# Kernel tuning notes

Measured on AMD Instinct MI355X. Metric: run time of the kernel, lower is better.

The kernel has to match this reference:

```python
import jax, jax.numpy as jnp
import numpy as np

NUM_HEADS = 16
HEAD_SIZE = 64
N_EMBED = 1024
BLOCK_SIZE = 1024
BATCH = 8


def setup_inputs() -> dict:
    key = jax.random.key(0)
    ks = jax.random.split(key, 8)
    s_in = 1.0 / np.sqrt(N_EMBED)
    x = jax.random.normal(ks[0], (BATCH, BLOCK_SIZE, N_EMBED), dtype=jnp.float32)
    Wq = jax.random.normal(ks[1], (N_EMBED, N_EMBED), dtype=jnp.float32) * s_in
    Wk = jax.random.normal(ks[2], (N_EMBED, N_EMBED), dtype=jnp.float32) * s_in
    Wv = jax.random.normal(ks[3], (N_EMBED, N_EMBED), dtype=jnp.float32) * s_in
    Wo = jax.random.normal(ks[4], (N_EMBED, N_EMBED), dtype=jnp.float32) * s_in
    bo = jnp.zeros((N_EMBED,), dtype=jnp.float32)
    W1 = jax.random.normal(ks[5], (N_EMBED, N_EMBED), dtype=jnp.float32) * s_in
    b1 = jnp.zeros((N_EMBED,), dtype=jnp.float32)
    return {"x": x, "Wq": Wq, "Wk": Wk, "Wv": Wv, "Wo": Wo, "bo": bo, "W1": W1, "b1": b1}


def reference(x, Wq, Wk, Wv, Wo, bo, W1, b1):
    B, T, E = x.shape
    H, Dh = NUM_HEADS, HEAD_SIZE
    # per-head projections (bias=False), concatenated weights reshaped to heads
    q = (x @ Wq).reshape(B, T, H, Dh)
    k = (x @ Wk).reshape(B, T, H, Dh)
    v = (x @ Wv).reshape(B, T, H, Dh)
    scale = Dh ** -0.5
    scores = jnp.einsum("bqhd,bkhd->bhqk", q, k) * scale  # [B,H,T,T]
    causal = jnp.tril(jnp.ones((T, T), dtype=bool))
    scores = jnp.where(causal, scores, jnp.float32(-jnp.inf))
    attn = jax.nn.softmax(scores, axis=-1)
    out = jnp.einsum("bhqk,bkhd->bqhd", attn, v).reshape(B, T, E)
    out = out @ Wo + bo  # output projection
    # FeedForward: Linear(E, E) + ReLU
    out = jax.nn.relu(out @ W1 + b1)
    return out
```

## Files before the change

### kernel.cpp

```cpp
#include <hip/hip_runtime.h>

typedef __bf16 bf16x8 __attribute__((ext_vector_type(8)));
typedef float f32x4 __attribute__((ext_vector_type(4)));
typedef short short4v __attribute__((ext_vector_type(4)));
typedef short short8v __attribute__((ext_vector_type(8)));

#define DEVI static __device__ __forceinline__

DEVI short f2bf(float f) {
    union { __bf16 b; short s; } u;
    u.b = (__bf16)f;
    return u.s;
}

DEVI void gld16(const void* g, void* l) {
    __builtin_amdgcn_global_load_lds(
        (const __attribute__((address_space(1))) unsigned int*)g,
        (__attribute__((address_space(3))) unsigned int*)l, 16, 0, 0);
}

__global__ __launch_bounds__(256) void cvt_x_kernel(const float* __restrict__ x,
                                                    short* __restrict__ xb) {
    int i = (blockIdx.x * 256 + threadIdx.x) * 8;
    f32x4 a = *(const f32x4*)(x + i);
    f32x4 b = *(const f32x4*)(x + i + 4);
    short8v o;
    o[0]=f2bf(a[0]); o[1]=f2bf(a[1]); o[2]=f2bf(a[2]); o[3]=f2bf(a[3]);
    o[4]=f2bf(b[0]); o[5]=f2bf(b[1]); o[6]=f2bf(b[2]); o[7]=f2bf(b[3]);
    *(short8v*)(xb + i) = o;
}

__global__ __launch_bounds__(256) void wtrans5_kernel(const float* __restrict__ w0,
                                                      const float* __restrict__ w1,
                                                      const float* __restrict__ w2,
                                                      const float* __restrict__ w3,
                                                      const float* __restrict__ w4,
                                                      short* __restrict__ dst) {
    const float* w;
    switch (blockIdx.z) {
        case 0: w = w0; break;
        case 1: w = w1; break;
        case 2: w = w2; break;
        case 3: w = w3; break;
        default: w = w4; break;
    }
    short* wt = dst + (size_t)blockIdx.z * 1048576;
    __shared__ float t[64][68];
    const int tid = threadIdx.x;
    const int k0 = blockIdx.x * 64, n0 = blockIdx.y * 64;
#pragma unroll
    for (int it = 0; it < 4; ++it) {
        int r = (tid >> 4) + it * 16;
        int cc = (tid & 15) * 4;
        f32x4 vv = *(const f32x4*)(w + (k0 + r) * 1024 + n0 + cc);
        *(f32x4*)&t[r][cc] = vv;
    }
    __syncthreads();
    if (blockIdx.z == 3) {
#pragma unroll
        for (int it = 0; it < 4; ++it) {
            int r = (tid >> 4) + it * 16;
            int cc = (tid & 15) * 4;
            short4v o;
            o[0] = f2bf(t[r][cc + 0]);
            o[1] = f2bf(t[r][cc + 1]);
            o[2] = f2bf(t[r][cc + 2]);
            o[3] = f2bf(t[r][cc + 3]);
            *(short4v*)(wt + (k0 + r) * 1024 + n0 + cc) = o;
        }
    } else {
#pragma unroll
        for (int it = 0; it < 4; ++it) {
            int n = (tid >> 4) + it * 16;
            int kc = (tid & 15) * 4;
            short4v o;
            o[0] = f2bf(t[kc + 0][n]);
            o[1] = f2bf(t[kc + 1][n]);
            o[2] = f2bf(t[kc + 2][n]);
            o[3] = f2bf(t[kc + 3][n]);
            *(short4v*)(wt + (n0 + n) * 1024 + k0 + kc) = o;
        }
    }
}

__global__ __launch_bounds__(256) void bcomb_kernel(const float* __restrict__ bo,
                                                    const float* __restrict__ W1,
                                                    const float* __restrict__ b1,
                                                    float* __restrict__ out) {
    __shared__ f32x4 red[64][4];
    const int tid = threadIdx.x;
    const int jg = tid >> 2;
    const int nq = tid & 3;
    const int n = blockIdx.x * 16 + nq * 4;
    f32x4 acc = {0.f, 0.f, 0.f, 0.f};
#pragma unroll 4
    for (int jj = 0; jj < 16; ++jj) {
        int j = jg * 16 + jj;
        float s = bo[j];
        f32x4 w = *(const f32x4*)(W1 + j * 1024 + n);
        acc[0] += s * w[0]; acc[1] += s * w[1]; acc[2] += s * w[2]; acc[3] += s * w[3];
    }
    red[jg][nq] = acc;
    __syncthreads();
#pragma unroll
    for (int s = 32; s >= 1; s >>= 1) {
        if (jg < s) {
            f32x4 a = red[jg][nq], b2 = red[jg + s][nq];
            a[0] += b2[0]; a[1] += b2[1]; a[2] += b2[2]; a[3] += b2[3];
            red[jg][nq] = a;
        }
        __syncthreads();
    }
    if (jg == 0) {
        f32x4 r = red[0][nq];
        f32x4 bb = *(const f32x4*)(b1 + n);
        r[0] += bb[0]; r[1] += bb[1]; r[2] += bb[2]; r[3] += bb[3];
        *(f32x4*)(out + n) = r;
    }
}

__global__ __launch_bounds__(256, 2) void gemm64_bt(const short* __restrict__ A,
                                                    const short* __restrict__ Bt,
                                                    short* __restrict__ outp) {
    __shared__ short As[64 * 64];
    __shared__ short Bs[64 * 64];
    const int tid = threadIdx.x;
    const int lane = tid & 63;
    const int wid = tid >> 6;
    const int g = lane >> 4, c = lane & 15;
    const int wr = wid >> 1, wc = wid & 1;
    const int m0 = blockIdx.x * 64, n0 = blockIdx.y * 64;

    const f32x4 fz = {0.f, 0.f, 0.f, 0.f};
    f32x4 acc[2][2];
#pragma unroll
    for (int m = 0; m < 2; ++m)
#pragma unroll
        for (int n = 0; n < 2; ++n) acc[m][n] = fz;

    for (int kt = 0; kt < 16; ++kt) {
        const int k0 = kt * 64;
        __syncthreads();
#pragma unroll
        for (int st = 0; st < 2; ++st) {
            int ci = st * 256 + tid;
            int r = ci >> 3;
            int cc = ((ci & 7) ^ (r & 7)) << 3;
            gld16(A + (m0 + r) * 1024 + k0 + cc, (char*)As + ci * 16);
            gld16(Bt + (n0 + r) * 1024 + k0 + cc, (char*)Bs + ci * 16);
        }
        __syncthreads();
#pragma unroll
        for (int kk = 0; kk < 2; ++kk) {
            bf16x8 af[2], bfr[2];
#pragma unroll
            for (int m = 0; m < 2; ++m) {
                int row = wr * 32 + m * 16 + c;
                af[m] = *(const bf16x8*)((const char*)As + row * 128 + ((kk * 64 + g * 16) ^ ((row & 7) << 4)));
            }
#pragma unroll
            for (int n = 0; n < 2; ++n) {
                int row = wc * 32 + n * 16 + c;
                bfr[n] = *(const bf16x8*)((const char*)Bs + row * 128 + ((kk * 64 + g * 16) ^ ((row & 7) << 4)));
            }
#pragma unroll
            for (int m = 0; m < 2; ++m)
#pragma unroll
                for (int n = 0; n < 2; ++n)
                    acc[m][n] = __builtin_amdgcn_mfma_f32_16x16x32_bf16(af[m], bfr[n], acc[m][n], 0, 0, 0);
        }
    }

#pragma unroll
    for (int n = 0; n < 2; ++n) {
        const int col = n0 + wc * 32 + n * 16 + c;
#pragma unroll
        for (int m = 0; m < 2; ++m) {
            const int row0 = m0 + wr * 32 + m * 16 + g * 4;
#pragma unroll
            for (int i = 0; i < 4; ++i)
                outp[(row0 + i) * 1024 + col] = f2bf(acc[m][n][i]);
        }
    }
}

template<int MODE>
__global__ __launch_bounds__(256, 2) void gemm_bt(const short* __restrict__ A,
                                                  const short* __restrict__ Bt,
                                                  const float* __restrict__ bias,
                                                  void* __restrict__ outp) {
    __shared__ short As[128 * 64];
    __shared__ short Bs[128 * 64];
    const int tid = threadIdx.x;
    const int lane = tid & 63;
    const int wid = tid >> 6;
    const int g = lane >> 4, c = lane & 15;
    const int wr = wid >> 1, wc = wid & 1;
    const int m0 = blockIdx.x * 128, n0 = blockIdx.y * 128;

    const f32x4 fz = {0.f, 0.f, 0.f, 0.f};
    f32x4 acc[4][4];
#pragma unroll
    for (int m = 0; m < 4; ++m)
#pragma unroll
        for (int n = 0; n < 4; ++n) acc[m][n] = fz;

    for (int kt = 0; kt < 16; ++kt) {
        const int k0 = kt * 64;
        __syncthreads();
#pragma unroll
        for (int st = 0; st < 4; ++st) {
            int ci = st * 256 + tid;
            int r = ci >> 3;
            int cc = ((ci & 7) ^ (r & 7)) << 3;
            gld16(A + (m0 + r) * 1024 + k0 + cc, (char*)As + ci * 16);
            gld16(Bt + (n0 + r) * 1024 + k0 + cc, (char*)Bs + ci * 16);
        }
        __syncthreads();
#pragma unroll
        for (int kk = 0; kk < 2; ++kk) {
            bf16x8 af[4], bfr[4];
#pragma unroll
            for (int m = 0; m < 4; ++m) {
                int row = wr * 64 + m * 16 + c;
                af[m] = *(const bf16x8*)((const char*)As + row * 128 + ((kk * 64 + g * 16) ^ ((row & 7) << 4)));
            }
#pragma unroll
            for (int n = 0; n < 4; ++n) {
                int row = wc * 64 + n * 16 + c;
                bfr[n] = *(const bf16x8*)((const char*)Bs + row * 128 + ((kk * 64 + g * 16) ^ ((row & 7) << 4)));
            }
#pragma unroll
            for (int m = 0; m < 4; ++m)
#pragma unroll
                for (int n = 0; n < 4; ++n)
                    acc[m][n] = __builtin_amdgcn_mfma_f32_16x16x32_bf16(af[m], bfr[n], acc[m][n], 0, 0, 0);
        }
    }

#pragma unroll
    for (int n = 0; n < 4; ++n) {
        const int col = n0 + wc * 64 + n * 16 + c;
        float bv = 0.f;
        if (MODE == 2) bv = bias[col];
#pragma unroll
        for (int m = 0; m < 4; ++m) {
            const int row0 = m0 + wr * 64 + m * 16 + g * 4;
#pragma unroll
            for (int i = 0; i < 4; ++i) {
                const int row = row0 + i;
                float val = acc[m][n][i];
                if (MODE == 0) {
                    short* qkv = (short*)outp;
                    int which = col >> 10;
                    int hc = col & 1023;
                    if (which == 0) val *= 0.18033688011112042f;
                    int dst = which * 8388608 +
                              (((row >> 10) * 16 + (hc >> 6)) * 1024 + (row & 1023)) * 64 + (hc & 63);
                    qkv[dst] = f2bf(val);
                } else {
                    ((float*)outp)[row * 1024 + col] = fmaxf(val + bv, 0.f);
                }
            }
        }
    }
}

__global__ __launch_bounds__(512, 2) void attn_kernel(const short* __restrict__ qp,
                                                      const short* __restrict__ kp,
                                                      const short* __restrict__ vp,
                                                      short* __restrict__ ao) {
    __shared__ short Ks[128 * 64];
    __shared__ short Vt[64 * 128];
    __shared__ short Ps[8][16 * 64];
    const int tid = threadIdx.x;
    const int lane = tid & 63;
    const int wid = tid >> 6;
    const int g = lane >> 4, c = lane & 15;
    const int bh = blockIdx.y;
    const int base = bh * 65536;
    const int b = bh >> 4, h = bh & 15;

    const int r0 = tid >> 3, c0 = (tid & 7) << 3;
    const int r1 = 64 + r0;
    const int vt0 = (tid >> 4) * 4;
    const int vd0 = (tid & 15) * 4;

    const f32x4 fz = {0.f, 0.f, 0.f, 0.f};

    bf16x8 kreg0, kreg1;
    short4v vreg0, vreg1, vreg2, vreg3;

#pragma unroll 1
    for (int ph = 0; ph < 2; ++ph) {
        const int qt = ph ? (7 - blockIdx.x) : blockIdx.x;
        const int q0 = qt * 128;
        const int nkt = qt + 1;

        const int qrow = q0 + wid * 16 + c;
        bf16x8 qf0 = *(const bf16x8*)(qp + base + qrow * 64 + g * 8);
        bf16x8 qf1 = *(const bf16x8*)(qp + base + qrow * 64 + 32 + g * 8);

        f32x4 accO[4];
#pragma unroll
        for (int n = 0; n < 4; ++n) accO[n] = fz;
        float mrow[4], lsum[4];
#pragma unroll
        for (int i = 0; i < 4; ++i) { mrow[i] = -1e30f; lsum[i] = 0.f; }

        kreg0 = *(const bf16x8*)(kp + base + r0 * 64 + c0);
        kreg1 = *(const bf16x8*)(kp + base + r1 * 64 + c0);
        vreg0 = *(const short4v*)(vp + base + (vt0 + 0) * 64 + vd0);
        vreg1 = *(const short4v*)(vp + base + (vt0 + 1) * 64 + vd0);
        vreg2 = *(const short4v*)(vp + base + (vt0 + 2) * 64 + vd0);
        vreg3 = *(const short4v*)(vp + base + (vt0 + 3) * 64 + vd0);

        for (int kt = 0; kt < nkt; ++kt) {
            __syncthreads();
            *(bf16x8*)((char*)Ks + r0 * 128 + ((c0 * 2) ^ ((r0 & 7) << 4))) = kreg0;
            *(bf16x8*)((char*)Ks + r1 * 128 + ((c0 * 2) ^ ((r1 & 7) << 4))) = kreg1;
#pragma unroll
            for (int i = 0; i < 4; ++i) {
                short4v w; w[0] = vreg0[i]; w[1] = vreg1[i]; w[2] = vreg2[i]; w[3] = vreg3[i];
                int d = vd0 + i;
                int swz = ((d & 7) ^ (d >> 3)) << 4;
                *(short4v*)((char*)Vt + d * 256 + ((vt0 * 2) ^ swz)) = w;
            }
            if (kt + 1 < nkt) {
                const short* kp2 = kp + base + (kt + 1) * 8192;
                const short* vp2 = vp + base + (kt + 1) * 8192;
                kreg0 = *(const bf16x8*)(kp2 + r0 * 64 + c0);
                kreg1 = *(const bf16x8*)(kp2 + r1 * 64 + c0);
                vreg0 = *(const short4v*)(vp2 + (vt0 + 0) * 64 + vd0);
                vreg1 = *(const short4v*)(vp2 + (vt0 + 1) * 64 + vd0);
                vreg2 = *(const short4v*)(vp2 + (vt0 + 2) * 64 + vd0);
                vreg3 = *(const short4v*)(vp2 + (vt0 + 3) * 64 + vd0);
            }
            __syncthreads();

            const bool diag = (kt == nkt - 1);
            const int nlim = diag ? (wid + 1) : 8;

            f32x4 s[8];
            __builtin_amdgcn_s_setprio(1);
#pragma unroll
            for (int n = 0; n < 8; ++n) {
                s[n] = fz;
                if (n < nlim) {
                    int row = n * 16 + c;
                    int swz = (row & 7) << 4;
                    bf16x8 kf0 = *(const bf16x8*)((const char*)Ks + row * 128 + ((g * 16) ^ swz));
                    bf16x8 kf1 = *(const bf16x8*)((const char*)Ks + row * 128 + ((64 + g * 16) ^ swz));
                    s[n] = __builtin_amdgcn_mfma_f32_16x16x32_bf16(qf0, kf0, s[n], 0, 0, 0);
                    s[n] = __builtin_amdgcn_mfma_f32_16x16x32_bf16(qf1, kf1, s[n], 0, 0, 0);
                }
            }
            __builtin_amdgcn_s_setprio(0);

            const int qg0 = q0 + wid * 16 + g * 4;
            float pm[4];
#pragma unroll
            for (int i = 0; i < 4; ++i) pm[i] = -1e30f;
            if (diag) {
#pragma unroll
                for (int n = 0; n < 8; ++n) {
                    int kg = kt * 128 + n * 16 + c;
#pragma unroll
                    for (int i = 0; i < 4; ++i) {
                        float vv = s[n][i];
                        vv = (kg <= qg0 + i) ? vv : -1e30f;
                        s[n][i] = vv;
                        pm[i] = fmaxf(pm[i], vv);
                    }
                }
            } else {
#pragma unroll
                for (int n = 0; n < 8; ++n)
#pragma unroll
                    for (int i = 0; i < 4; ++i)
                        pm[i] = fmaxf(pm[i], s[n][i]);
            }
#pragma unroll
            for (int off = 1; off < 16; off <<= 1)
#pragma unroll
                for (int i = 0; i < 4; ++i)
                    pm[i] = fmaxf(pm[i], __shfl_xor(pm[i], off));

            int need = 0;
#pragma unroll
            for (int i = 0; i < 4; ++i) need |= (pm[i] > mrow[i] + 8.f) ? 1 : 0;
            if (__any(need)) {
#pragma unroll
                for (int i = 0; i < 4; ++i) {
                    float mnew = fmaxf(mrow[i], pm[i]);
                    float corr = exp2f(mrow[i] - mnew);
                    mrow[i] = mnew;
                    lsum[i] *= corr;
#pragma unroll
                    for (int n = 0; n < 4; ++n) accO[n][i] *= corr;
                }
            }
#pragma unroll
            for (int n = 0; n < 8; ++n)
#pragma unroll
                for (int i = 0; i < 4; ++i) {
                    float pv = exp2f(s[n][i] - mrow[i]);
                    s[n][i] = pv;
                    lsum[i] += pv;
                }

#pragma unroll
            for (int hf = 0; hf < 2; ++hf) {
                asm volatile("s_waitcnt lgkmcnt(0)" ::: "memory");
                __builtin_amdgcn_sched_barrier(0);
#pragma unroll
                for (int n4 = 0; n4 < 4; ++n4) {
                    int tl = n4 * 16 + c;
#pragma unroll
                    for (int i = 0; i < 4; ++i) {
                        int q = g * 4 + i;
                        *(short*)((char*)&Ps[wid][0] + q * 128 + ((tl * 2) ^ ((q & 7) << 4))) =
                            f2bf(s[hf * 4 + n4][i]);
                    }
                }
                asm volatile("s_waitcnt lgkmcnt(0)" ::: "memory");
                __builtin_amdgcn_sched_barrier(0);
#pragma unroll
                for (int ksl = 0; ksl < 2; ++ksl) {
                    const int ks = hf * 2 + ksl;
                    bf16x8 paf = *(const bf16x8*)((const char*)&Ps[wid][0] +
                                                  c * 128 + ((ksl * 64 + g * 16) ^ ((c & 7) << 4)));
                    __builtin_amdgcn_s_setprio(1);
#pragma unroll
                    for (int n = 0; n < 4; ++n) {
                        int d = n * 16 + c;
                        int swz = ((d & 7) ^ (d >> 3)) << 4;
                        bf16x8 vf = *(const bf16x8*)((const char*)Vt + d * 256 + ((ks * 64 + g * 16) ^ swz));
                        accO[n] = __builtin_amdgcn_mfma_f32_16x16x32_bf16(paf, vf, accO[n], 0, 0, 0);
                    }
                    __builtin_amdgcn_s_setprio(0);
                }
            }
        }

        float lrow[4];
#pragma unroll
        for (int i = 0; i < 4; ++i) lrow[i] = lsum[i];
#pragma unroll
        for (int off = 1; off < 16; off <<= 1)
#pragma unroll
            for (int i = 0; i < 4; ++i)
                lrow[i] += __shfl_xor(lrow[i], off);
        float inv[4];
#pragma unroll
        for (int i = 0; i < 4; ++i) inv[i] = __builtin_amdgcn_rcpf(lrow[i]);
#pragma unroll
        for (int n = 0; n < 4; ++n)
#pragma unroll
            for (int i = 0; i < 4; ++i) {
                int t = q0 + wid * 16 + g * 4 + i;
                float o = accO[n][i] * inv[i];
                ao[(b * 1024 + t) * 1024 + h * 64 + n * 16 + c] = f2bf(o);
            }
    }
}

extern "C" void kernel_launch(void* const* d_in, const int* in_sizes, int n_in,
                              void* d_out, int out_size, void* d_ws, size_t ws_size,
                              hipStream_t stream) {
    const float* x  = (const float*)d_in[0];
    const float* Wq = (const float*)d_in[1];
    const float* Wk = (const float*)d_in[2];
    const float* Wv = (const float*)d_in[3];
    const float* Wo = (const float*)d_in[4];
    const float* bo = (const float*)d_in[5];
    const float* W1 = (const float*)d_in[6];
    const float* b1 = (const float*)d_in[7];

    char* ws = (char*)d_ws;
    short* xb    = (short*)(ws + 0);
    short* wallT = (short*)(ws + 16777216);
    short* qb    = (short*)(ws + 27262976);
    short* kb    = qb + 8388608;
    short* vb    = qb + 16777216;
    short* ao    = xb;
    short* wqkvT = wallT;
    short* woBF  = wallT + 3145728;
    short* w1T   = wallT + 4194304;
    short* wcombT= wqkvT;
    float* bcomb = (float*)(ws + 16777216 + 2097152);

    cvt_x_kernel<<<4096, 256, 0, stream>>>(x, xb);
    wtrans5_kernel<<<dim3(16, 16, 5), 256, 0, stream>>>(Wq, Wk, Wv, Wo, W1, wallT);

    gemm_bt<0><<<dim3(64, 24), 256, 0, stream>>>(xb, wqkvT, nullptr, (void*)qb);
    gemm64_bt<<<dim3(16, 16), 256, 0, stream>>>(w1T, woBF, wcombT);
    bcomb_kernel<<<64, 256, 0, stream>>>(bo, W1, b1, bcomb);
    attn_kernel<<<dim3(4, 128), 512, 0, stream>>>(qb, kb, vb, ao);
    gemm_bt<2><<<dim3(64, 8), 256, 0, stream>>>(ao, wcombT, bcomb, d_out);
}
```

Baseline: 167.5 us.

## Restructure attention to 4 waves with 32 query rows each and 64-key tiles

The attention kernel moves from 8 waves of 16 query rows to 4 waves of 32 query rows, and from 128-key tiles to 64-key tiles. Each K/V fragment read from LDS is now reused across two MFMA row groups, which lowers LDS traffic per FLOP, and the finer key tiles trim wasted work on the causal diagonal. The cost is more accumulator registers per lane, fewer waves per block, and twice as many barrier-synchronised tile iterations.

New measurement: 172.6 us. 3.0% more time.

```diff
diff --git a/kernel.cpp b/kernel.cpp
--- a/kernel.cpp
+++ b/kernel.cpp
@@ -266,13 +266,13 @@
     }
 }
 
-__global__ __launch_bounds__(512, 2) void attn_kernel(const short* __restrict__ qp,
+__global__ __launch_bounds__(256, 2) void attn_kernel(const short* __restrict__ qp,
                                                       const short* __restrict__ kp,
                                                       const short* __restrict__ vp,
                                                       short* __restrict__ ao) {
-    __shared__ short Ks[128 * 64];
-    __shared__ short Vt[64 * 128];
-    __shared__ short Ps[8][16 * 64];
+    __shared__ short Ks[64 * 64];
+    __shared__ short Vt[64 * 64];
+    __shared__ short Ps[4][32 * 64];
     const int tid = threadIdx.x;
     const int lane = tid & 63;
     const int wid = tid >> 6;
@@ -282,7 +282,6 @@
     const int b = bh >> 4, h = bh & 15;
 
     const int r0 = tid >> 3, c0 = (tid & 7) << 3;
-    const int r1 = 64 + r0;
     const int vt0 = (tid >> 4) * 4;
     const int vd0 = (tid & 15) * 4;
 
@@ -295,21 +294,29 @@
     for (int ph = 0; ph < 2; ++ph) {
         const int qt = ph ? (7 - blockIdx.x) : blockIdx.x;
         const int q0 = qt * 128;
-        const int nkt = qt + 1;
-
-        const int qrow = q0 + wid * 16 + c;
-        bf16x8 qf0 = *(const bf16x8*)(qp + base + qrow * 64 + g * 8);
-        bf16x8 qf1 = *(const bf16x8*)(qp + base + qrow * 64 + 32 + g * 8);
-
-        f32x4 accO[4];
-#pragma unroll
-        for (int n = 0; n < 4; ++n) accO[n] = fz;
-        float mrow[4], lsum[4];
-#pragma unroll
-        for (int i = 0; i < 4; ++i) { mrow[i] = -1e30f; lsum[i] = 0.f; }
+        const int nkt = (qt + 1) * 2;
+        const int qlo = q0 + wid * 32;
+
+        bf16x8 qf[2][2];
+#pragma unroll
+        for (int m = 0; m < 2; ++m)
+#pragma unroll
+            for (int hh = 0; hh < 2; ++hh)
+                qf[m][hh] = *(const bf16x8*)(qp + base + (qlo + m * 16 + c) * 64 + hh * 32 + g * 8);
+
+        f32x4 accO[2][4];
+#pragma unroll
+        for (int m = 0; m < 2; ++m)
+#pragma unroll
+            for (int n = 0; n < 4; ++n) accO[m][n] = fz;
+        float mrow[2][4], lsum[2][4];
+#pragma unroll
+        for (int m = 0; m < 2; ++m)
+#pragma unroll
+            for (int i = 0; i < 4; ++i) { mrow[m][i] = -1e30f; lsum[m][i] = 0.f; }
 
         kreg0 = *(const bf16x8*)(kp + base + r0 * 64 + c0);
-        kreg1 = *(const bf16x8*)(kp + base + r1 * 64 + c0);
+        kreg1 = *(const bf16x8*)(kp + base + (r0 + 32) * 64 + c0);
         vreg0 = *(const short4v*)(vp + base + (vt0 + 0) * 64 + vd0);
         vreg1 = *(const short4v*)(vp + base + (vt0 + 1) * 64 + vd0);
         vreg2 = *(const short4v*)(vp + base + (vt0 + 2) * 64 + vd0);
@@ -318,19 +325,18 @@
         for (int kt = 0; kt < nkt; ++kt) {
             __syncthreads();
             *(bf16x8*)((char*)Ks + r0 * 128 + ((c0 * 2) ^ ((r0 & 7) << 4))) = kreg0;
-            *(bf16x8*)((char*)Ks + r1 * 128 + ((c0 * 2) ^ ((r1 & 7) << 4))) = kreg1;
+            *(bf16x8*)((char*)Ks + (r0 + 32) * 128 + ((c0 * 2) ^ ((r0 & 7) << 4))) = kreg1;
 #pragma unroll
             for (int i = 0; i < 4; ++i) {
                 short4v w; w[0] = vreg0[i]; w[1] = vreg1[i]; w[2] = vreg2[i]; w[3] = vreg3[i];
                 int d = vd0 + i;
-                int swz = ((d & 7) ^ (d >> 3)) << 4;
-                *(short4v*)((char*)Vt + d * 256 + ((vt0 * 2) ^ swz)) = w;
+                *(short4v*)((char*)Vt + d * 128 + ((vt0 * 2) ^ ((d & 7) << 4))) = w;
             }
             if (kt + 1 < nkt) {
-                const short* kp2 = kp + base + (kt + 1) * 8192;
-                const short* vp2 = vp + base + (kt + 1) * 8192;
+                const short* kp2 = kp + base + (kt + 1) * 4096;
+                const short* vp2 = vp + base + (kt + 1) * 4096;
                 kreg0 = *(const bf16x8*)(kp2 + r0 * 64 + c0);
-                kreg1 = *(const bf16x8*)(kp2 + r1 * 64 + c0);
+                kreg1 = *(const bf16x8*)(kp2 + (r0 + 32) * 64 + c0);
                 vreg0 = *(const short4v*)(vp2 + (vt0 + 0) * 64 + vd0);
                 vreg1 = *(const short4v*)(vp2 + (vt0 + 1) * 64 + vd0);
                 vreg2 = *(const short4v*)(vp2 + (vt0 + 2) * 64 + vd0);
@@ -338,130 +344,165 @@
             }
             __syncthreads();
 
-            const bool diag = (kt == nkt - 1);
-            const int nlim = diag ? (wid + 1) : 8;
-
-            f32x4 s[8];
-            __builtin_amdgcn_s_setprio(1);
-#pragma unroll
-            for (int n = 0; n < 8; ++n) {
-                s[n] = fz;
-                if (n < nlim) {
-                    int row = n * 16 + c;
-                    int swz = (row & 7) << 4;
-                    bf16x8 kf0 = *(const bf16x8*)((const char*)Ks + row * 128 + ((g * 16) ^ swz));
-                    bf16x8 kf1 = *(const bf16x8*)((const char*)Ks + row * 128 + ((64 + g * 16) ^ swz));
-                    s[n] = __builtin_amdgcn_mfma_f32_16x16x32_bf16(qf0, kf0, s[n], 0, 0, 0);
-                    s[n] = __builtin_amdgcn_mfma_f32_16x16x32_bf16(qf1, kf1, s[n], 0, 0, 0);
-                }
-            }
-            __builtin_amdgcn_s_setprio(0);
-
-            const int qg0 = q0 + wid * 16 + g * 4;
-            float pm[4];
-#pragma unroll
-            for (int i = 0; i < 4; ++i) pm[i] = -1e30f;
-            if (diag) {
-#pragma unroll
-                for (int n = 0; n < 8; ++n) {
-                    int kg = kt * 128 + n * 16 + c;
-#pragma unroll
-                    for (int i = 0; i < 4; ++i) {
-                        float vv = s[n][i];
-                        vv = (kg <= qg0 + i) ? vv : -1e30f;
-                        s[n][i] = vv;
-                        pm[i] = fmaxf(pm[i], vv);
+            const int klo = kt * 64;
+            const bool skip = klo > qlo + 31;
+            if (!skip) {
+                const bool needMask = (klo + 63 > qlo);
+                int nlim = 4;
+                if (needMask) {
+                    nlim = ((qlo + 31 - klo) >> 4) + 1;
+                    if (nlim > 4) nlim = 4;
+                }
+
+                f32x4 s[2][4];
+#pragma unroll
+                for (int m = 0; m < 2; ++m)
+#pragma unroll
+                    for (int n = 0; n < 4; ++n) s[m][n] = fz;
+                __builtin_amdgcn_s_setprio(1);
+#pragma unroll
+                for (int n = 0; n < 4; ++n) {
+                    if (n < nlim) {
+                        int row = n * 16 + c;
+                        int swz = (c & 7) << 4;
+                        bf16x8 kf0 = *(const bf16x8*)((const char*)Ks + row * 128 + ((g * 16) ^ swz));
+                        bf16x8 kf1 = *(const bf16x8*)((const char*)Ks + row * 128 + ((64 + g * 16) ^ swz));
+#pragma unroll
+                        for (int m = 0; m < 2; ++m) {
+                            s[m][n] = __builtin_amdgcn_mfma_f32_16x16x32_bf16(qf[m][0], kf0, s[m][n], 0, 0, 0);
+                            s[m][n] = __builtin_amdgcn_mfma_f32_16x16x32_bf16(qf[m][1], kf1, s[m][n], 0, 0, 0);
+                        }
                     }
                 }
-            } else {
-#pragma unroll
-                for (int n = 0; n < 8; ++n)
+                __builtin_amdgcn_s_setprio(0);
+
+                float pm[2][4];
+#pragma unroll
+                for (int m = 0; m < 2; ++m)
+#pragma unroll
+                    for (int i = 0; i < 4; ++i) pm[m][i] = -1e30f;
+                if (needMask) {
+#pragma unroll
+                    for (int n = 0; n < 4; ++n) {
+                        int kg = klo + n * 16 + c;
+#pragma unroll
+                        for (int m = 0; m < 2; ++m)
+#pragma unroll
+                            for (int i = 0; i < 4; ++i) {
+                                float vv = s[m][n][i];
+                                vv = (kg <= qlo + m * 16 + g * 4 + i) ? vv : -1e30f;
+                                s[m][n][i] = vv;
+                                pm[m][i] = fmaxf(pm[m][i], vv);
+                            }
+                    }
+                } else {
+#pragma unroll
+                    for (int n = 0; n < 4; ++n)
+#pragma unroll
+                        for (int m = 0; m < 2; ++m)
+#pragma unroll
+                            for (int i = 0; i < 4; ++i)
+                                pm[m][i] = fmaxf(pm[m][i], s[m][n][i]);
+                }
+#pragma unroll
+                for (int off = 1; off < 16; off <<= 1)
+#pragma unroll
+                    for (int m = 0; m < 2; ++m)
+#pragma unroll
+                        for (int i = 0; i < 4; ++i)
+                            pm[m][i] = fmaxf(pm[m][i], __shfl_xor(pm[m][i], off));
+
+                int need = 0;
+#pragma unroll
+                for (int m = 0; m < 2; ++m)
 #pragma unroll
                     for (int i = 0; i < 4; ++i)
-                        pm[i] = fmaxf(pm[i], s[n][i]);
-            }
-#pragma unroll
-            for (int off = 1; off < 16; off <<= 1)
-#pragma unroll
-                for (int i = 0; i < 4; ++i)
-                    pm[i] = fmaxf(pm[i], __shfl_xor(pm[i], off));
-
-            int need = 0;
-#pragma unroll
-            for (int i = 0; i < 4; ++i) need |= (pm[i] > mrow[i] + 8.f) ? 1 : 0;
-            if (__any(need)) {
-#pragma unroll
-                for (int i = 0; i < 4; ++i) {
-                    float mnew = fmaxf(mrow[i], pm[i]);
-                    float corr = exp2f(mrow[i] - mnew);
-                    mrow[i] = mnew;
-                    lsum[i] *= corr;
-#pragma unroll
-                    for (int n = 0; n < 4; ++n) accO[n][i] *= corr;
-                }
-            }
-#pragma unroll
-            for (int n = 0; n < 8; ++n)
-#pragma unroll
-                for (int i = 0; i < 4; ++i) {
-                    float pv = exp2f(s[n][i] - mrow[i]);
-                    s[n][i] = pv;
-                    lsum[i] += pv;
-                }
-
-#pragma unroll
-            for (int hf = 0; hf < 2; ++hf) {
+                        need |= (pm[m][i] > mrow[m][i] + 8.f) ? 1 : 0;
+                if (__any(need)) {
+#pragma unroll
+                    for (int m = 0; m < 2; ++m)
+#pragma unroll
+                        for (int i = 0; i < 4; ++i) {
+                            float mnew = fmaxf(mrow[m][i], pm[m][i]);
+                            float corr = exp2f(mrow[m][i] - mnew);
+                            mrow[m][i] = mnew;
+                            lsum[m][i] *= corr;
+#pragma unroll
+                            for (int n = 0; n < 4; ++n) accO[m][n][i] *= corr;
+                        }
+                }
+#pragma unroll
+                for (int m = 0; m < 2; ++m)
+#pragma unroll
+                    for (int n = 0; n < 4; ++n)
+#pragma unroll
+                        for (int i = 0; i < 4; ++i) {
+                            float pv = exp2f(s[m][n][i] - mrow[m][i]);
+                            s[m][n][i] = pv;
+                            lsum[m][i] += pv;
+                        }
+
                 asm volatile("s_waitcnt lgkmcnt(0)" ::: "memory");
                 __builtin_amdgcn_sched_barrier(0);
 #pragma unroll
-                for (int n4 = 0; n4 < 4; ++n4) {
-                    int tl = n4 * 16 + c;
-#pragma unroll
-                    for (int i = 0; i < 4; ++i) {
-                        int q = g * 4 + i;
-                        *(short*)((char*)&Ps[wid][0] + q * 128 + ((tl * 2) ^ ((q & 7) << 4))) =
-                            f2bf(s[hf * 4 + n4][i]);
+                for (int m = 0; m < 2; ++m)
+#pragma unroll
+                    for (int n = 0; n < 4; ++n) {
+                        int t = n * 16 + c;
+#pragma unroll
+                        for (int i = 0; i < 4; ++i) {
+                            int q = m * 16 + g * 4 + i;
+                            *(short*)((char*)&Ps[wid][0] + q * 128 + ((t * 2) ^ ((q & 7) << 4))) =
+                                f2bf(s[m][n][i]);
+                        }
                     }
-                }
                 asm volatile("s_waitcnt lgkmcnt(0)" ::: "memory");
                 __builtin_amdgcn_sched_barrier(0);
-#pragma unroll
-                for (int ksl = 0; ksl < 2; ++ksl) {
-                    const int ks = hf * 2 + ksl;
-                    bf16x8 paf = *(const bf16x8*)((const char*)&Ps[wid][0] +
-                                                  c * 128 + ((ksl * 64 + g * 16) ^ ((c & 7) << 4)));
+
+#pragma unroll
+                for (int kk = 0; kk < 2; ++kk) {
+                    bf16x8 paf[2];
+#pragma unroll
+                    for (int m = 0; m < 2; ++m)
+                        paf[m] = *(const bf16x8*)((const char*)&Ps[wid][0] +
+                                                  (m * 16 + c) * 128 + ((kk * 64 + g * 16) ^ ((c & 7) << 4)));
                     __builtin_amdgcn_s_setprio(1);
 #pragma unroll
                     for (int n = 0; n < 4; ++n) {
                         int d = n * 16 + c;
-                        int swz = ((d & 7) ^ (d >> 3)) << 4;
-                        bf16x8 vf = *(const bf16x8*)((const char*)Vt + d * 256 + ((ks * 64 + g * 16) ^ swz));
-                        accO[n] = __builtin_amdgcn_mfma_f32_16x16x32_bf16(paf, vf, accO[n], 0, 0, 0);
+                        bf16x8 vf = *(const bf16x8*)((const char*)Vt + d * 128 +
+                                                     ((kk * 64 + g * 16) ^ ((d & 7) << 4)));
+#pragma unroll
+                        for (int m = 0; m < 2; ++m)
+                            accO[m][n] = __builtin_amdgcn_mfma_f32_16x16x32_bf16(paf[m], vf, accO[m][n], 0, 0, 0);
                     }
                     __builtin_amdgcn_s_setprio(0);
                 }
             }
         }
 
-        float lrow[4];
-#pragma unroll
-        for (int i = 0; i < 4; ++i) lrow[i] = lsum[i];
-#pragma unroll
-        for (int off = 1; off < 16; off <<= 1)
-#pragma unroll
-            for (int i = 0; i < 4; ++i)
-                lrow[i] += __shfl_xor(lrow[i], off);
-        float inv[4];
-#pragma unroll
-        for (int i = 0; i < 4; ++i) inv[i] = __builtin_amdgcn_rcpf(lrow[i]);
-#pragma unroll
-        for (int n = 0; n < 4; ++n)
-#pragma unroll
-            for (int i = 0; i < 4; ++i) {
-                int t = q0 + wid * 16 + g * 4 + i;
-                float o = accO[n][i] * inv[i];
-                ao[(b * 1024 + t) * 1024 + h * 64 + n * 16 + c] = f2bf(o);
-            }
+#pragma unroll
+        for (int m = 0; m < 2; ++m) {
+            float lrow[4];
+#pragma unroll
+            for (int i = 0; i < 4; ++i) lrow[i] = lsum[m][i];
+#pragma unroll
+            for (int off = 1; off < 16; off <<= 1)
+#pragma unroll
+                for (int i = 0; i < 4; ++i)
+                    lrow[i] += __shfl_xor(lrow[i], off);
+            float inv[4];
+#pragma unroll
+            for (int i = 0; i < 4; ++i) inv[i] = __builtin_amdgcn_rcpf(lrow[i]);
+#pragma unroll
+            for (int n = 0; n < 4; ++n)
+#pragma unroll
+                for (int i = 0; i < 4; ++i) {
+                    int t = qlo + m * 16 + g * 4 + i;
+                    float o = accO[m][n][i] * inv[i];
+                    ao[(b * 1024 + t) * 1024 + h * 64 + n * 16 + c] = f2bf(o);
+                }
+        }
     }
 }
 
@@ -496,6 +537,6 @@
     gemm_bt<0><<<dim3(64, 24), 256, 0, stream>>>(xb, wqkvT, nullptr, (void*)qb);
     gemm64_bt<<<dim3(16, 16), 256, 0, stream>>>(w1T, woBF, wcombT);
     bcomb_kernel<<<64, 256, 0, stream>>>(bo, W1, b1, bcomb);
-    attn_kernel<<<dim3(4, 128), 512, 0, stream>>>(qb, kb, vb, ao);
+    attn_kernel<<<dim3(4, 128), 256, 0, stream>>>(qb, kb, vb, ao);
     gemm_bt<2><<<dim3(64, 8), 256, 0, stream>>>(ao, wcombT, bcomb, d_out);
 }
```
